# Kernel optimization log

Measured on AMD Instinct MI355X. Metric: run time of the kernel, lower is better.

## Reference

```python
import jax, jax.numpy as jnp
import numpy as np

B = 8192
N_COLS = 64
D = 1024
EPS = 1e-5


def _layernorm(x, g, b):
    m = jnp.mean(x, axis=-1, keepdims=True)
    v = jnp.mean(jnp.square(x - m), axis=-1, keepdims=True)
    return (x - m) * jax.lax.rsqrt(v + EPS) * g + b


def setup_inputs() -> dict:
    key = jax.random.key(0)
    ks = jax.random.split(key, 8)
    s = 0.02
    return {
        "x1_enc": jax.random.normal(ks[0], (1, N_COLS, D), jnp.float32),
        "x2_enc": jax.random.normal(ks[1], (B, D), jnp.float32),
        "We": jax.random.normal(ks[2], (4, 2 * D, D), jnp.float32) * s,
        "be": jnp.zeros((4, D), jnp.float32),
        "W1": jax.random.normal(ks[3], (2 * D, 4 * D), jnp.float32) * s,
        "b1": jnp.zeros((4 * D,), jnp.float32),
        "g1": jnp.ones((4 * D,), jnp.float32),
        "bt1": jnp.zeros((4 * D,), jnp.float32),
        "W2": jax.random.normal(ks[4], (4 * D, 2 * D), jnp.float32) * s,
        "b2": jnp.zeros((2 * D,), jnp.float32),
        "g2": jnp.ones((2 * D,), jnp.float32),
        "bt2": jnp.zeros((2 * D,), jnp.float32),
        "W3": jax.random.normal(ks[5], (2 * D, 1), jnp.float32) * s,
        "b3": jnp.zeros((1,), jnp.float32),
        "col_pairs": jax.random.randint(ks[6], (B, 2), 0, N_COLS, jnp.int64),
        "vis_type": jax.random.randint(ks[7], (B,), 0, 4, jnp.int64),
    }


def reference(x1_enc, x2_enc, We, be, W1, b1, g1, bt1, W2, b2, g2, bt2, W3, b3,
              col_pairs, vis_type):
    # x1 repeated B times is identical per row -> gather directly from x1_enc[0]
    x11 = x1_enc[0, col_pairs[:, 0]]          # [B, D]
    x12 = x1_enc[0, col_pairs[:, 1]]          # [B, D]
    x1c = jnp.concatenate([x11, x12], axis=1)  # [B, 2D]

    # 1-of-4 expert routing: compute all experts, select by vis_type
    all_y = jax.nn.relu(jnp.einsum('bd,edk->bek', x1c, We) + be)  # [B, 4, D]
    y1 = jnp.take_along_axis(all_y, vis_type[:, None, None], axis=1)[:, 0]  # [B, D]

    y = jnp.concatenate([y1, x2_enc], axis=1)  # [B, 2D]
    h = _layernorm(jax.nn.relu(y @ W1 + b1), g1, bt1)
    h = _layernorm(jax.nn.relu(h @ W2 + b2), g2, bt2)
    return jax.nn.sigmoid(h @ W3 + b3)  # [B, 1]
```

## Files before the change

### kernel.cpp

```cpp
#include <hip/hip_runtime.h>

typedef unsigned short u16;
typedef __bf16 bf16x8 __attribute__((ext_vector_type(8)));
typedef float f32x4v __attribute__((ext_vector_type(4)));
typedef u16 u16x8 __attribute__((ext_vector_type(8)));

__device__ __forceinline__ u16 f2bf(float f) {
  union { float f; unsigned u; } v; v.f = f;
  unsigned r = v.u + 0x7fffu + ((v.u >> 16) & 1u);
  return (u16)(r >> 16);
}
__device__ __forceinline__ float bf2f(u16 h) {
  union { unsigned u; float f; } v; v.u = ((unsigned)h) << 16;
  return v.f;
}

#define G2L16(g, l)                                                            \
  __builtin_amdgcn_global_load_lds((__attribute__((address_space(1))) void*)(g), \
                                   (__attribute__((address_space(3))) void*)(l), 16, 0, 0)

__global__ __launch_bounds__(256) void k_transpose2(const float* __restrict__ W1,
                                                    u16* __restrict__ W1T,
                                                    const float* __restrict__ W2,
                                                    u16* __restrict__ W2T) {
  __shared__ float tile[64][65];
  int bid = blockIdx.x;
  const float* in;
  u16* out;
  int R, C, bx, by;
  if (bid < 2048) {
    in = W1; out = W1T; R = 2048; C = 4096;
    bx = bid & 63; by = bid >> 6;
  } else {
    bid -= 2048;
    in = W2; out = W2T; R = 4096; C = 2048;
    bx = bid & 31; by = bid >> 5;
  }
  const int c0 = bx * 64, r0 = by * 64;
  const int tc = (threadIdx.x & 15) * 4, tr = threadIdx.x >> 4;
#pragma unroll
  for (int i = 0; i < 4; ++i) {
    int r = tr + i * 16;
    f32x4v v = *(const f32x4v*)(in + (size_t)(r0 + r) * C + c0 + tc);
    tile[r][tc] = v[0]; tile[r][tc + 1] = v[1];
    tile[r][tc + 2] = v[2]; tile[r][tc + 3] = v[3];
  }
  __syncthreads();
  const int oc = threadIdx.x >> 2;
  const int rb = (threadIdx.x & 3) * 16;
  u16x8 o0, o1;
#pragma unroll
  for (int i = 0; i < 8; ++i) o0[i] = f2bf(tile[rb + i][oc]);
#pragma unroll
  for (int i = 0; i < 8; ++i) o1[i] = f2bf(tile[rb + 8 + i][oc]);
  *(u16x8*)(out + (size_t)(c0 + oc) * R + r0 + rb) = o0;
  *(u16x8*)(out + (size_t)(c0 + oc) * R + r0 + rb + 8) = o1;
}

__global__ __launch_bounds__(256) void k_pq(const float* __restrict__ x1,
                                            const float* __restrict__ We,
                                            float* __restrict__ pq) {
  const int n0 = blockIdx.x * 64;
  const int ep = blockIdx.y;
  const int e = ep >> 1, p = ep & 1;
  const int ks = blockIdx.z * 128;
  __shared__ float As[64][33];
  __shared__ float Bs[32][68];
  const int t = threadIdx.x;
  const int tx = t & 15, ty = t >> 4;
  float acc[4][4] = {};
  const float* wbase = We + (size_t)e * 2048 * 1024 + (size_t)p * 1024 * 1024;
  for (int k0 = ks; k0 < ks + 128; k0 += 32) {
#pragma unroll
    for (int i = 0; i < 8; ++i) {
      int idx = t + i * 256;
      As[idx >> 5][idx & 31] = x1[(size_t)(idx >> 5) * 1024 + k0 + (idx & 31)];
    }
#pragma unroll
    for (int i = 0; i < 8; ++i) {
      int idx = t + i * 256;
      Bs[idx >> 6][idx & 63] = wbase[(size_t)(k0 + (idx >> 6)) * 1024 + n0 + (idx & 63)];
    }
    __syncthreads();
#pragma unroll
    for (int kk = 0; kk < 32; ++kk) {
      float av[4];
#pragma unroll
      for (int i = 0; i < 4; ++i) av[i] = As[ty * 4 + i][kk];
      f32x4v bv = *(const f32x4v*)&Bs[kk][tx * 4];
#pragma unroll
      for (int i = 0; i < 4; ++i)
#pragma unroll
        for (int j = 0; j < 4; ++j) acc[i][j] += av[i] * bv[j];
    }
    __syncthreads();
  }
#pragma unroll
  for (int i = 0; i < 4; ++i) {
    float* dst = pq + ((size_t)ep * 64 + ty * 4 + i) * 1024 + n0 + tx * 4;
#pragma unroll
    for (int j = 0; j < 4; ++j) atomicAdd(&dst[j], acc[i][j]);
  }
}

__global__ __launch_bounds__(256) void k_build_y(const float* __restrict__ pq,
                                                 const float* __restrict__ x2,
                                                 const float* __restrict__ be,
                                                 const int* __restrict__ cp,
                                                 const int* __restrict__ vis,
                                                 u16* __restrict__ Y) {
  const int b = blockIdx.x;
  const int t = threadIdx.x;
  const int e = vis[b];
  u16x8 o;
  if (t < 128) {
    const int c0 = cp[2 * b], c1 = cp[2 * b + 1];
    const float* P = pq + ((size_t)(e * 2) * 64 + c0) * 1024 + t * 8;
    const float* Q = pq + ((size_t)(e * 2 + 1) * 64 + c1) * 1024 + t * 8;
    const float* B = be + e * 1024 + t * 8;
#pragma unroll
    for (int i = 0; i < 8; ++i) {
      float v = P[i] + Q[i] + B[i];
      o[i] = f2bf(v > 0.f ? v : 0.f);
    }
    *(u16x8*)(Y + (size_t)b * 2048 + t * 8) = o;
  } else {
    const float* X = x2 + (size_t)b * 1024 + (size_t)(t - 128) * 8;
#pragma unroll
    for (int i = 0; i < 8; ++i) o[i] = f2bf(X[i]);
    *(u16x8*)(Y + (size_t)b * 2048 + 1024 + (size_t)(t - 128) * 8) = o;
  }
}

__global__ __launch_bounds__(256, 3) void k_gemm(const u16* __restrict__ A,
                                                 const u16* __restrict__ BT,
                                                 const float* __restrict__ bias,
                                                 u16* __restrict__ C, int M, int N, int K) {
  __shared__ u16 As[128 * 64];
  __shared__ u16 Bs[128 * 64];
  const int tid = threadIdx.x;
  const int lane = tid & 63;
  const int wave = tid >> 6;

  const int nx = gridDim.x, ny = gridDim.y;
  const int bid = blockIdx.y * nx + blockIdx.x;
  const int stripe = ny >> 3;
  const int xcd = bid & 7;
  const int loc = bid >> 3;
  const int panel = loc / (stripe * 4);
  const int rem = loc - panel * (stripe * 4);
  const int by = xcd * stripe + (rem >> 2);
  const int bx = panel * 4 + (rem & 3);
  const int tileN = bx * 128;
  const int tileM = by * 128;
  const int wm = wave & 1;
  const int wn = wave >> 1;

  f32x4v acc[4][4];
#pragma unroll
  for (int i = 0; i < 4; ++i)
#pragma unroll
    for (int j = 0; j < 4; ++j) acc[i][j] = (f32x4v){0.f, 0.f, 0.f, 0.f};

  const int srow = tid >> 3;
  const int lchunk = (tid & 7) ^ (srow & 7);
  const u16* aptr = A + (size_t)(tileM + srow) * K + lchunk * 8;
  const u16* bptr = BT + (size_t)(tileN + srow) * K + lchunk * 8;
  u16* asp = As + tid * 8;
  u16* bsp = Bs + tid * 8;

  const int s = lane & 7;
  const int kp0 = ((lane >> 4) ^ s) * 8;
  const int kp1 = kp0 ^ 32;
  const int am = wm * 64 + (lane & 15);
  const int bn = wn * 64 + (lane & 15);

  for (int k0 = 0; k0 < K; k0 += 64) {
    G2L16(aptr, asp);
    G2L16(aptr + (size_t)32 * K, asp + 2048);
    G2L16(aptr + (size_t)64 * K, asp + 4096);
    G2L16(aptr + (size_t)96 * K, asp + 6144);
    G2L16(bptr, bsp);
    G2L16(bptr + (size_t)32 * K, bsp + 2048);
    G2L16(bptr + (size_t)64 * K, bsp + 4096);
    G2L16(bptr + (size_t)96 * K, bsp + 6144);
    aptr += 64;
    bptr += 64;
    __syncthreads();

    bf16x8 af[4], bfr[4];
#pragma unroll
    for (int mi = 0; mi < 4; ++mi)
      af[mi] = *(const bf16x8*)(As + (am + mi * 16) * 64 + kp0);
#pragma unroll
    for (int ni = 0; ni < 4; ++ni)
      bfr[ni] = *(const bf16x8*)(Bs + (bn + ni * 16) * 64 + kp0);
#pragma unroll
    for (int mi = 0; mi < 4; ++mi)
#pragma unroll
      for (int ni = 0; ni < 4; ++ni)
        acc[mi][ni] = __builtin_amdgcn_mfma_f32_16x16x32_bf16(af[mi], bfr[ni], acc[mi][ni], 0, 0, 0);
#pragma unroll
    for (int mi = 0; mi < 4; ++mi)
      af[mi] = *(const bf16x8*)(As + (am + mi * 16) * 64 + kp1);
#pragma unroll
    for (int ni = 0; ni < 4; ++ni)
      bfr[ni] = *(const bf16x8*)(Bs + (bn + ni * 16) * 64 + kp1);
#pragma unroll
    for (int mi = 0; mi < 4; ++mi)
#pragma unroll
      for (int ni = 0; ni < 4; ++ni)
        acc[mi][ni] = __builtin_amdgcn_mfma_f32_16x16x32_bf16(af[mi], bfr[ni], acc[mi][ni], 0, 0, 0);
    __syncthreads();
  }

  const int crow = tileM + wm * 64 + (lane >> 4) * 4;
  const int ccol = tileN + wn * 64 + (lane & 15);
#pragma unroll
  for (int mi = 0; mi < 4; ++mi) {
#pragma unroll
    for (int ni = 0; ni < 4; ++ni) {
      const int c = ccol + ni * 16;
      const float bv = bias[c];
      const int r0 = crow + mi * 16;
#pragma unroll
      for (int r = 0; r < 4; ++r) {
        float v = acc[mi][ni][r] + bv;
        v = v > 0.f ? v : 0.f;
        C[(size_t)(r0 + r) * N + c] = f2bf(v);
      }
    }
  }
}

template <int CHUNKS>
__global__ __launch_bounds__(256) void k_ln(u16* __restrict__ H, const float* __restrict__ g,
                                            const float* __restrict__ bt) {
  const int cols = CHUNKS * 2048;
  u16* row = H + (size_t)blockIdx.x * cols;
  const int t = threadIdx.x;
  float vals[CHUNKS][8];
  float s = 0.f, ss = 0.f;
#pragma unroll
  for (int j = 0; j < CHUNKS; ++j) {
    u16x8 v = *(const u16x8*)(row + j * 2048 + t * 8);
#pragma unroll
    for (int i = 0; i < 8; ++i) {
      float f = bf2f(v[i]);
      vals[j][i] = f;
      s += f;
      ss += f * f;
    }
  }
#pragma unroll
  for (int off = 32; off > 0; off >>= 1) {
    s += __shfl_down(s, off, 64);
    ss += __shfl_down(ss, off, 64);
  }
  __shared__ float red[8];
  const int lane = t & 63, wv = t >> 6;
  if (lane == 0) { red[wv] = s; red[4 + wv] = ss; }
  __syncthreads();
  if (t == 0) {
    float S = red[0] + red[1] + red[2] + red[3];
    float SS = red[4] + red[5] + red[6] + red[7];
    float m = S * (1.f / cols);
    float var = SS * (1.f / cols) - m * m;
    red[0] = m;
    red[1] = rsqrtf(var + 1e-5f);
  }
  __syncthreads();
  const float m = red[0], rs = red[1];
#pragma unroll
  for (int j = 0; j < CHUNKS; ++j) {
    u16x8 o;
#pragma unroll
    for (int i = 0; i < 8; ++i) {
      int col = j * 2048 + t * 8 + i;
      o[i] = f2bf((vals[j][i] - m) * rs * g[col] + bt[col]);
    }
    *(u16x8*)(row + j * 2048 + t * 8) = o;
  }
}

__global__ __launch_bounds__(256) void k_ln_final(const u16* __restrict__ H2,
                                                  const float* __restrict__ g,
                                                  const float* __restrict__ bt,
                                                  const float* __restrict__ W3,
                                                  const float* __restrict__ b3,
                                                  float* __restrict__ out) {
  const int b = blockIdx.x, t = threadIdx.x;
  const u16* row = H2 + (size_t)b * 2048;
  float vals[8];
  float s = 0.f, ss = 0.f;
  {
    u16x8 v = *(const u16x8*)(row + t * 8);
#pragma unroll
    for (int i = 0; i < 8; ++i) {
      float f = bf2f(v[i]);
      vals[i] = f;
      s += f;
      ss += f * f;
    }
  }
#pragma unroll
  for (int off = 32; off > 0; off >>= 1) {
    s += __shfl_down(s, off, 64);
    ss += __shfl_down(ss, off, 64);
  }
  __shared__ float red[8];
  const int lane = t & 63, wv = t >> 6;
  if (lane == 0) { red[wv] = s; red[4 + wv] = ss; }
  __syncthreads();
  if (t == 0) {
    float S = red[0] + red[1] + red[2] + red[3];
    float SS = red[4] + red[5] + red[6] + red[7];
    float m = S * (1.f / 2048.f);
    float var = SS * (1.f / 2048.f) - m * m;
    red[0] = m;
    red[1] = rsqrtf(var + 1e-5f);
  }
  __syncthreads();
  const float m = red[0], rs = red[1];
  float dot = 0.f;
#pragma unroll
  for (int i = 0; i < 8; ++i) {
    int col = t * 8 + i;
    float h = (vals[i] - m) * rs * g[col] + bt[col];
    dot += h * W3[col];
  }
#pragma unroll
  for (int off = 32; off > 0; off >>= 1) dot += __shfl_down(dot, off, 64);
  __syncthreads();
  if (lane == 0) red[wv] = dot;
  __syncthreads();
  if (t == 0) {
    float S = red[0] + red[1] + red[2] + red[3] + b3[0];
    out[b] = 1.f / (1.f + expf(-S));
  }
}

extern "C" void kernel_launch(void* const* d_in, const int* in_sizes, int n_in,
                              void* d_out, int out_size, void* d_ws, size_t ws_size,
                              hipStream_t stream) {
  const float* x1 = (const float*)d_in[0];
  const float* x2 = (const float*)d_in[1];
  const float* We = (const float*)d_in[2];
  const float* be = (const float*)d_in[3];
  const float* W1 = (const float*)d_in[4];
  const float* b1 = (const float*)d_in[5];
  const float* g1 = (const float*)d_in[6];
  const float* bt1 = (const float*)d_in[7];
  const float* W2 = (const float*)d_in[8];
  const float* b2 = (const float*)d_in[9];
  const float* g2 = (const float*)d_in[10];
  const float* bt2 = (const float*)d_in[11];
  const float* W3 = (const float*)d_in[12];
  const float* b3 = (const float*)d_in[13];
  const int* cp = (const int*)d_in[14];
  const int* vis = (const int*)d_in[15];
  float* out = (float*)d_out;

  char* ws = (char*)d_ws;
  u16* W1T = (u16*)(ws);
  u16* W2T = (u16*)(ws + 16777216);
  u16* Y   = (u16*)(ws + 33554432);
  u16* H1  = (u16*)(ws + 67108864);
  float* PQ = (float*)(ws + 134217728);
  u16* H2 = Y;

  hipMemsetAsync(PQ, 0, 8 * 64 * 1024 * sizeof(float), stream);
  k_transpose2<<<4096, 256, 0, stream>>>(W1, W1T, W2, W2T);
  k_pq<<<dim3(16, 8, 8), 256, 0, stream>>>(x1, We, PQ);
  k_build_y<<<8192, 256, 0, stream>>>(PQ, x2, be, cp, vis, Y);
  k_gemm<<<dim3(4096 / 128, 8192 / 128), 256, 0, stream>>>(Y, W1T, b1, H1, 8192, 4096, 2048);
  k_ln<2><<<8192, 256, 0, stream>>>(H1, g1, bt1);
  k_gemm<<<dim3(2048 / 128, 8192 / 128), 256, 0, stream>>>(H1, W2T, b2, H2, 8192, 2048, 4096);
  k_ln_final<<<8192, 256, 0, stream>>>(H2, g2, bt2, W3, b3, out);
}
```

Baseline: 516.3 us.

## Fold first LayerNorm into second GEMM epilogue via per-row stats

```diff
diff --git a/kernel.cpp b/kernel.cpp
--- a/kernel.cpp
+++ b/kernel.cpp
@@ -22,18 +22,19 @@
 __global__ __launch_bounds__(256) void k_transpose2(const float* __restrict__ W1,
                                                     u16* __restrict__ W1T,
                                                     const float* __restrict__ W2,
-                                                    u16* __restrict__ W2T) {
+                                                    u16* __restrict__ W2gT,
+                                                    const float* __restrict__ g1) {
   __shared__ float tile[64][65];
   int bid = blockIdx.x;
   const float* in;
   u16* out;
-  int R, C, bx, by;
+  int R, C, bx, by, fold;
   if (bid < 2048) {
-    in = W1; out = W1T; R = 2048; C = 4096;
+    in = W1; out = W1T; R = 2048; C = 4096; fold = 0;
     bx = bid & 63; by = bid >> 6;
   } else {
     bid -= 2048;
-    in = W2; out = W2T; R = 4096; C = 2048;
+    in = W2; out = W2gT; R = 4096; C = 2048; fold = 1;
     bx = bid & 31; by = bid >> 5;
   }
   const int c0 = bx * 64, r0 = by * 64;
@@ -48,29 +49,34 @@
   __syncthreads();
   const int oc = threadIdx.x >> 2;
   const int rb = (threadIdx.x & 3) * 16;
+  float gv[16];
+#pragma unroll
+  for (int i = 0; i < 16; ++i) gv[i] = fold ? g1[r0 + rb + i] : 1.f;
   u16x8 o0, o1;
 #pragma unroll
-  for (int i = 0; i < 8; ++i) o0[i] = f2bf(tile[rb + i][oc]);
-#pragma unroll
-  for (int i = 0; i < 8; ++i) o1[i] = f2bf(tile[rb + 8 + i][oc]);
+  for (int i = 0; i < 8; ++i) o0[i] = f2bf(tile[rb + i][oc] * gv[i]);
+#pragma unroll
+  for (int i = 0; i < 8; ++i) o1[i] = f2bf(tile[rb + 8 + i][oc] * gv[8 + i]);
   *(u16x8*)(out + (size_t)(c0 + oc) * R + r0 + rb) = o0;
   *(u16x8*)(out + (size_t)(c0 + oc) * R + r0 + rb + 8) = o1;
 }
 
 __global__ __launch_bounds__(256) void k_pq(const float* __restrict__ x1,
                                             const float* __restrict__ We,
-                                            float* __restrict__ pq) {
+                                            float* __restrict__ pq0,
+                                            float* __restrict__ pq1) {
   const int n0 = blockIdx.x * 64;
   const int ep = blockIdx.y;
   const int e = ep >> 1, p = ep & 1;
-  const int ks = blockIdx.z * 128;
+  const int ks = blockIdx.z * 512;
+  float* pq = blockIdx.z ? pq1 : pq0;
   __shared__ float As[64][33];
   __shared__ float Bs[32][68];
   const int t = threadIdx.x;
   const int tx = t & 15, ty = t >> 4;
   float acc[4][4] = {};
   const float* wbase = We + (size_t)e * 2048 * 1024 + (size_t)p * 1024 * 1024;
-  for (int k0 = ks; k0 < ks + 128; k0 += 32) {
+  for (int k0 = ks; k0 < ks + 512; k0 += 32) {
 #pragma unroll
     for (int i = 0; i < 8; ++i) {
       int idx = t + i * 256;
@@ -99,11 +105,31 @@
   for (int i = 0; i < 4; ++i) {
     float* dst = pq + ((size_t)ep * 64 + ty * 4 + i) * 1024 + n0 + tx * 4;
 #pragma unroll
-    for (int j = 0; j < 4; ++j) atomicAdd(&dst[j], acc[i][j]);
-  }
-}
-
-__global__ __launch_bounds__(256) void k_build_y(const float* __restrict__ pq,
+    for (int j = 0; j < 4; ++j) dst[j] = acc[i][j];
+  }
+}
+
+__global__ __launch_bounds__(256) void k_w2vec(const float* __restrict__ W2,
+                                               const float* __restrict__ g1,
+                                               const float* __restrict__ bt1,
+                                               const float* __restrict__ b2,
+                                               float* __restrict__ s1,
+                                               float* __restrict__ c1b) {
+  const int n = blockIdx.x * 256 + threadIdx.x;
+  const int ks = blockIdx.y * 256;
+  float s = 0.f, c = 0.f;
+  for (int k = ks; k < ks + 256; ++k) {
+    float w = W2[(size_t)k * 2048 + n];
+    s += g1[k] * w;
+    c += bt1[k] * w;
+  }
+  if (blockIdx.y == 0) c += b2[n];
+  atomicAdd(&s1[n], s);
+  atomicAdd(&c1b[n], c);
+}
+
+__global__ __launch_bounds__(256) void k_build_y(const float* __restrict__ pq0,
+                                                 const float* __restrict__ pq1,
                                                  const float* __restrict__ x2,
                                                  const float* __restrict__ be,
                                                  const int* __restrict__ cp,
@@ -115,12 +141,12 @@
   u16x8 o;
   if (t < 128) {
     const int c0 = cp[2 * b], c1 = cp[2 * b + 1];
-    const float* P = pq + ((size_t)(e * 2) * 64 + c0) * 1024 + t * 8;
-    const float* Q = pq + ((size_t)(e * 2 + 1) * 64 + c1) * 1024 + t * 8;
+    const size_t po = ((size_t)(e * 2) * 64 + c0) * 1024 + t * 8;
+    const size_t qo = ((size_t)(e * 2 + 1) * 64 + c1) * 1024 + t * 8;
     const float* B = be + e * 1024 + t * 8;
 #pragma unroll
     for (int i = 0; i < 8; ++i) {
-      float v = P[i] + Q[i] + B[i];
+      float v = pq0[po + i] + pq1[po + i] + pq0[qo + i] + pq1[qo + i] + B[i];
       o[i] = f2bf(v > 0.f ? v : 0.f);
     }
     *(u16x8*)(Y + (size_t)b * 2048 + t * 8) = o;
@@ -132,9 +158,13 @@
   }
 }
 
-__global__ __launch_bounds__(256, 3) void k_gemm(const u16* __restrict__ A,
+template <int MODE>
+__global__ __launch_bounds__(256, 4) void k_gemm(const u16* __restrict__ A,
                                                  const u16* __restrict__ BT,
                                                  const float* __restrict__ bias,
+                                                 const float2* __restrict__ stats,
+                                                 const float* __restrict__ s1,
+                                                 const float* __restrict__ c1b,
                                                  u16* __restrict__ C, int M, int N, int K) {
   __shared__ u16 As[128 * 64];
   __shared__ u16 Bs[128 * 64];
@@ -216,38 +246,52 @@
 
   const int crow = tileM + wm * 64 + (lane >> 4) * 4;
   const int ccol = tileN + wn * 64 + (lane & 15);
+  float cv0[4], cv1[4];
+#pragma unroll
+  for (int ni = 0; ni < 4; ++ni) {
+    const int c = ccol + ni * 16;
+    if (MODE == 0) {
+      cv0[ni] = bias[c];
+    } else {
+      cv0[ni] = s1[c];
+      cv1[ni] = c1b[c];
+    }
+  }
 #pragma unroll
   for (int mi = 0; mi < 4; ++mi) {
 #pragma unroll
-    for (int ni = 0; ni < 4; ++ni) {
-      const int c = ccol + ni * 16;
-      const float bv = bias[c];
-      const int r0 = crow + mi * 16;
-#pragma unroll
-      for (int r = 0; r < 4; ++r) {
-        float v = acc[mi][ni][r] + bv;
+    for (int r = 0; r < 4; ++r) {
+      const int row = crow + mi * 16 + r;
+      float m = 0.f, rs = 0.f;
+      if (MODE == 1) {
+        float2 st = stats[row];
+        m = st.x; rs = st.y;
+      }
+#pragma unroll
+      for (int ni = 0; ni < 4; ++ni) {
+        float v;
+        if (MODE == 0)
+          v = acc[mi][ni][r] + cv0[ni];
+        else
+          v = rs * acc[mi][ni][r] - rs * m * cv0[ni] + cv1[ni];
         v = v > 0.f ? v : 0.f;
-        C[(size_t)(r0 + r) * N + c] = f2bf(v);
+        C[(size_t)row * N + ccol + ni * 16] = f2bf(v);
       }
     }
   }
 }
 
-template <int CHUNKS>
-__global__ __launch_bounds__(256) void k_ln(u16* __restrict__ H, const float* __restrict__ g,
-                                            const float* __restrict__ bt) {
-  const int cols = CHUNKS * 2048;
-  u16* row = H + (size_t)blockIdx.x * cols;
+__global__ __launch_bounds__(256) void k_stats(const u16* __restrict__ H1,
+                                               float2* __restrict__ stats) {
+  const u16* row = H1 + (size_t)blockIdx.x * 4096;
   const int t = threadIdx.x;
-  float vals[CHUNKS][8];
   float s = 0.f, ss = 0.f;
 #pragma unroll
-  for (int j = 0; j < CHUNKS; ++j) {
+  for (int j = 0; j < 2; ++j) {
     u16x8 v = *(const u16x8*)(row + j * 2048 + t * 8);
 #pragma unroll
     for (int i = 0; i < 8; ++i) {
       float f = bf2f(v[i]);
-      vals[j][i] = f;
       s += f;
       ss += f * f;
     }
@@ -264,22 +308,9 @@
   if (t == 0) {
     float S = red[0] + red[1] + red[2] + red[3];
     float SS = red[4] + red[5] + red[6] + red[7];
-    float m = S * (1.f / cols);
-    float var = SS * (1.f / cols) - m * m;
-    red[0] = m;
-    red[1] = rsqrtf(var + 1e-5f);
-  }
-  __syncthreads();
-  const float m = red[0], rs = red[1];
-#pragma unroll
-  for (int j = 0; j < CHUNKS; ++j) {
-    u16x8 o;
-#pragma unroll
-    for (int i = 0; i < 8; ++i) {
-      int col = j * 2048 + t * 8 + i;
-      o[i] = f2bf((vals[j][i] - m) * rs * g[col] + bt[col]);
-    }
-    *(u16x8*)(row + j * 2048 + t * 8) = o;
+    float m = S * (1.f / 4096.f);
+    float var = SS * (1.f / 4096.f) - m * m;
+    stats[blockIdx.x] = make_float2(m, rsqrtf(var + 1e-5f));
   }
 }
 
@@ -362,19 +393,26 @@
   float* out = (float*)d_out;
 
   char* ws = (char*)d_ws;
-  u16* W1T = (u16*)(ws);
-  u16* W2T = (u16*)(ws + 16777216);
-  u16* Y   = (u16*)(ws + 33554432);
-  u16* H1  = (u16*)(ws + 67108864);
-  float* PQ = (float*)(ws + 134217728);
+  u16* W1T  = (u16*)(ws);
+  u16* W2gT = (u16*)(ws + 16777216);
+  u16* Y    = (u16*)(ws + 33554432);
+  u16* H1   = (u16*)(ws + 67108864);
+  float* PQ0 = (float*)(ws + 134217728);
+  float* PQ1 = (float*)(ws + 136314880);
+  float2* stats = (float2*)(ws + 138412032);
+  float* s1  = (float*)(ws + 138477568);
+  float* c1b = (float*)(ws + 138485760);
   u16* H2 = Y;
 
-  hipMemsetAsync(PQ, 0, 8 * 64 * 1024 * sizeof(float), stream);
-  k_transpose2<<<4096, 256, 0, stream>>>(W1, W1T, W2, W2T);
-  k_pq<<<dim3(16, 8, 8), 256, 0, stream>>>(x1, We, PQ);
-  k_build_y<<<8192, 256, 0, stream>>>(PQ, x2, be, cp, vis, Y);
-  k_gemm<<<dim3(4096 / 128, 8192 / 128), 256, 0, stream>>>(Y, W1T, b1, H1, 8192, 4096, 2048);
-  k_ln<2><<<8192, 256, 0, stream>>>(H1, g1, bt1);
-  k_gemm<<<dim3(2048 / 128, 8192 / 128), 256, 0, stream>>>(H1, W2T, b2, H2, 8192, 2048, 4096);
+  hipMemsetAsync(s1, 0, 2 * 2048 * sizeof(float), stream);
+  k_transpose2<<<4096, 256, 0, stream>>>(W1, W1T, W2, W2gT, g1);
+  k_pq<<<dim3(16, 8, 2), 256, 0, stream>>>(x1, We, PQ0, PQ1);
+  k_w2vec<<<dim3(8, 16), 256, 0, stream>>>(W2, g1, bt1, b2, s1, c1b);
+  k_build_y<<<8192, 256, 0, stream>>>(PQ0, PQ1, x2, be, cp, vis, Y);
+  k_gemm<0><<<dim3(4096 / 128, 8192 / 128), 256, 0, stream>>>(
+      Y, W1T, b1, nullptr, nullptr, nullptr, H1, 8192, 4096, 2048);
+  k_stats<<<8192, 256, 0, stream>>>(H1, stats);
+  k_gemm<1><<<dim3(2048 / 128, 8192 / 128), 256, 0, stream>>>(
+      H1, W2gT, nullptr, stats, s1, c1b, H2, 8192, 2048, 4096);
   k_ln_final<<<8192, 256, 0, stream>>>(H2, g2, bt2, W3, b3, out);
 }
```

After: 491.7 us. 1.05x faster.
